# Kernel tuning notes

Measured on AMD Instinct MI355X. Metric: run time of the kernel, lower is better.

Reference implementation:

```python
import jax, jax.numpy as jnp
import numpy as np

B, L, T, IN, H, OUT = 1024, 64, 128, 13, 64, 13
NEG = -1e30


def gru_step(x, h, Wih, Whh, bih, bhh):
    # PyTorch GRU cell: gates ordered (r, z, n)
    gi = x @ Wih.T + bih          # [B, 3H]
    gh = h @ Whh.T + bhh          # [B, 3H]
    ir, iz, inn = jnp.split(gi, 3, axis=-1)
    hr, hz, hn = jnp.split(gh, 3, axis=-1)
    r = jax.nn.sigmoid(ir + hr)
    z = jax.nn.sigmoid(iz + hz)
    n = jnp.tanh(inn + r * hn)
    return (1.0 - z) * n + z * h


def setup_inputs() -> dict:
    key = jax.random.key(0)
    ks = jax.random.split(key, 10)
    s = float(1.0 / np.sqrt(H))
    x = jax.random.normal(ks[0], (B, L, IN), jnp.float32)
    lengths = jax.random.randint(ks[1], (B,), 1, L + 1).at[0].set(L)
    Wih = jax.random.uniform(ks[2], (3 * H, IN), jnp.float32, -s, s)
    Whh = jax.random.uniform(ks[3], (3 * H, H), jnp.float32, -s, s)
    bih = jax.random.uniform(ks[4], (3 * H,), jnp.float32, -s, s)
    bhh = jax.random.uniform(ks[5], (3 * H,), jnp.float32, -s, s)
    Wf = jax.random.uniform(ks[6], (OUT, H), jnp.float32, -s, s)
    bf = jax.random.uniform(ks[7], (OUT,), jnp.float32, -s, s)
    Wa = jax.random.uniform(ks[8], (H, H), jnp.float32, -s, s)
    ba = jax.random.uniform(ks[9], (H,), jnp.float32, -s, s)
    return dict(x=x, lengths=lengths, output_length=T, Wih=Wih, Whh=Whh,
                bih=bih, bhh=bhh, Wf=Wf, bf=bf, Wa=Wa, ba=ba)


def reference(x, lengths, output_length, Wih, Whh, bih, bhh, Wf, bf, Wa, ba):
    b, l = x.shape[0], x.shape[1]
    xT = jnp.swapaxes(x, 0, 1)                        # [L, B, IN]
    h0 = jnp.zeros((b, H), x.dtype)

    # Encoder: masked GRU emulating pack_padded/pad_packed semantics:
    # hidden frozen past each sequence's length; outputs zero past length.
    def enc(h, inp):
        t, xt = inp
        hn = gru_step(xt, h, Wih, Whh, bih, bhh)
        valid = (t < lengths)[:, None]
        h = jnp.where(valid, hn, h)
        return h, jnp.where(valid, hn, 0.0)

    h, outs = jax.lax.scan(enc, h0, (jnp.arange(l), xT))
    # output[:, -1, :] of the padded output (zeros for seqs shorter than max)
    nin = outs[-1] @ Wf.T + bf                        # [B, OUT]

    Tn = output_length
    buf0 = jnp.zeros((Tn, b, H), x.dtype)             # growing past-prediction buffer

    def dec(carry, t):
        h, buf, nin = carry
        hn = gru_step(nin, h, Wih, Whh, bih, bhh)     # output_lstm == hidden (1 layer, 1 step)
        # attention recomputed over all past predictions (softmax over time axis)
        logits = jnp.einsum('tbh,gh->tbg', buf, Wa) + ba      # [T, B, H]
        logits = jnp.where((jnp.arange(Tn) < t)[:, None, None], logits, NEG)
        w = jax.nn.softmax(logits, axis=0)
        o = hn + jnp.sum(w * buf, axis=0)             # at t=0 buffer is all zeros -> +0
        y = o @ Wf.T + bf
        return (hn, buf.at[t].set(o), y), y

    _, ys = jax.lax.scan(dec, (h, buf0, nin), jnp.arange(Tn))
    return jnp.swapaxes(ys, 0, 1)                     # [B, T, OUT]
```

## Files before the change

### kernel.cpp

```cpp
#include <hip/hip_runtime.h>
#include <stdint.h>
#include <math.h>

#define BATCH 1024
#define SEQL  64
#define TDEC  128
#define NIN   13
#define NH    64
#define NOUT  13

typedef _Float16 h2 __attribute__((ext_vector_type(2)));
typedef __fp16   g2 __attribute__((ext_vector_type(2)));

union FU  { uint32_t u; float f; };
union HU  { uint16_t u; _Float16 h; };
union H2U { uint32_t u; h2 h; g2 g; };

__device__ __forceinline__ float bf2f(uint16_t v) { FU t; t.u = ((uint32_t)v) << 16; return t.f; }
__device__ __forceinline__ float hf2f(uint16_t v) { HU t; t.u = v; return (float)t.h; }

__device__ __forceinline__ float ldf(const void* p, long i, int mode) {
    if (mode == 1) return bf2f(((const uint16_t*)p)[i]);
    if (mode == 2) return hf2f(((const uint16_t*)p)[i]);
    return ((const float*)p)[i];
}

__device__ __forceinline__ bool pass_stats(const void* p, int n, int lane, int mode,
                                           float band_lo, float band_hi, float max_ok) {
    int m = (n + 1) / 2;
    int cnt = (m < 64) ? m : 64;
    bool ok_max = true, in_band = false;
    if (lane < cnt) {
        long pos = 2L * (((long)lane * m) / cnt);
        float v = (mode == 1) ? bf2f(((const uint16_t*)p)[pos])
                              : hf2f(((const uint16_t*)p)[pos]);
        float a = fabsf(v);
        ok_max  = (a <= max_ok);
        in_band = (a >= band_lo && a <= band_hi);
    }
    bool allmax = __all(ok_max);
    int nb = (int)__popcll(__ballot(in_band));
    int need = cnt / 4; if (need < 1) need = 1;
    return allmax && (nb >= need);
}
__device__ __forceinline__ int detect(const void* p, int n, int lane,
                                      float band_lo, float band_hi, float max_ok) {
    if (pass_stats(p, n, lane, 1, band_lo, band_hi, max_ok)) return 1;
    if (pass_stats(p, n, lane, 2, band_lo, band_hi, max_ok)) return 2;
    return 0;
}
__device__ __forceinline__ bool detect_len64(const int* p, int lane) {
    int v = p[2 * lane + 1];
    return __all(v == 0);
}

__device__ __forceinline__ float dot2(h2 a, h2 b, float c) {
#if __has_builtin(__builtin_amdgcn_fdot2)
    return __builtin_amdgcn_fdot2(a, b, c, false);
#else
    return c + (float)a[0] * (float)b[0] + (float)a[1] * (float)b[1];
#endif
}
__device__ __forceinline__ uint32_t pku(float a, float b) {
    H2U t; t.g = __builtin_amdgcn_cvt_pkrtz(a, b); return t.u;
}
__device__ __forceinline__ h2 uh(uint32_t u) { H2U t; t.u = u; return t.h; }
__device__ __forceinline__ float rcp_(float x) { return __builtin_amdgcn_rcpf(x); }
__device__ __forceinline__ float exp2_(float x) {
#if __has_builtin(__builtin_amdgcn_exp2f)
    return __builtin_amdgcn_exp2f(x);
#else
    return __expf(x * 0.69314718056f);
#endif
}
__device__ __forceinline__ float sigm2(float xs)  { return rcp_(1.0f + exp2_(-xs)); }
__device__ __forceinline__ float tanh2(float xs)  { return 1.0f - 2.0f * rcp_(exp2_(xs) + 1.0f); }

__device__ __forceinline__ float swap1(float v) {
    FU a; a.f = v;
    FU b; b.u = (uint32_t)__builtin_amdgcn_mov_dpp((int)a.u, 0xB1, 0xF, 0xF, true);
    return b.f;
}

#define BCAST32(vreg, dst)                                                 \
    {                                                                      \
        uint32_t _pr = pku((vreg), swap1(vreg));                           \
        _Pragma("unroll")                                                  \
        for (int _k = 0; _k < 32; ++_k)                                    \
            (dst)[_k] = __builtin_amdgcn_readlane(_pr, 2 * _k);            \
    }

#define BWRITE(DSTB, V)                                                    \
    {                                                                      \
        float _w  = swap1(V);                                              \
        float _lo = odd ? _w  : (V);                                       \
        float _hi = odd ? (V) : _w;                                        \
        (DSTB)[jhalf] = pku(_lo, _hi);                                     \
    }
#define BREAD(SRC, DST)                                                    \
    {                                                                      \
        _Pragma("unroll")                                                  \
        for (int _k = 0; _k < 32; _k += 4) {                               \
            uint4 _q = *(const uint4*)((SRC) + _k);                        \
            (DST)[_k]     = _q.x; (DST)[_k + 1] = _q.y;                    \
            (DST)[_k + 2] = _q.z; (DST)[_k + 3] = _q.w;                    \
        }                                                                  \
    }

__global__ __launch_bounds__(64, 1)
void gru_attn_kernel(const void* __restrict__ x, const int* __restrict__ lengths,
                     const void* __restrict__ Wih, const void* __restrict__ Whh,
                     const void* __restrict__ bih, const void* __restrict__ bhh,
                     const void* __restrict__ Wf, const void* __restrict__ bfv,
                     const void* __restrict__ Wa, const void* __restrict__ ba,
                     float* __restrict__ out)
{
    const int b = blockIdx.x;
    const int j = threadIdx.x;
    const bool odd = j & 1;
    const int jhalf = j >> 1;

    __shared__ __align__(16) uint32_t ob[32];

    const int dX   = detect(x,   BATCH * SEQL * NIN, j, 0.25f, 4.0f, 16.0f);
    const int dWih = detect(Wih, 3 * NH * NIN, j, 0.04f, 0.13f, 0.14f);
    const int dWhh = detect(Whh, 3 * NH * NH,  j, 0.04f, 0.13f, 0.14f);
    const int dBih = detect(bih, 3 * NH,       j, 0.04f, 0.13f, 0.14f);
    const int dBhh = detect(bhh, 3 * NH,       j, 0.04f, 0.13f, 0.14f);
    const int dWf  = detect(Wf,  NOUT * NH,    j, 0.04f, 0.13f, 0.14f);
    const int dBf  = detect(bfv, NOUT,         j, 0.04f, 0.13f, 0.14f);
    const int dWa  = detect(Wa,  NH * NH,      j, 0.04f, 0.13f, 0.14f);
    const int dBa  = detect(ba,  NH,           j, 0.04f, 0.13f, 0.14f);
    const bool len64 = detect_len64(lengths, j);

    const float L2E  = 1.44269504089f;
    const float L2E2 = 2.88539008177f;

    h2 wihr[7], wihz[7], wihn[7];
    h2 whhr[32], whhz[32], whhn[32];
    h2 wap[32], wfp[32];

#pragma unroll
    for (int k = 0; k < 7; ++k) {
        float a0 = ldf(Wih, (0 * NH + j) * NIN + 2 * k, dWih);
        float a1 = (2 * k + 1 < NIN) ? ldf(Wih, (0 * NH + j) * NIN + 2 * k + 1, dWih) : 0.0f;
        wihr[k] = uh(pku(a0 * L2E, a1 * L2E));
        float b0 = ldf(Wih, (1 * NH + j) * NIN + 2 * k, dWih);
        float b1 = (2 * k + 1 < NIN) ? ldf(Wih, (1 * NH + j) * NIN + 2 * k + 1, dWih) : 0.0f;
        wihz[k] = uh(pku(b0 * L2E, b1 * L2E));
        float c0 = ldf(Wih, (2 * NH + j) * NIN + 2 * k, dWih);
        float c1 = (2 * k + 1 < NIN) ? ldf(Wih, (2 * NH + j) * NIN + 2 * k + 1, dWih) : 0.0f;
        wihn[k] = uh(pku(c0 * L2E2, c1 * L2E2));
    }
    const int jf = (j < NOUT) ? j : 0;
#pragma unroll
    for (int k = 0; k < 32; ++k) {
        whhr[k] = uh(pku(ldf(Whh, (0 * NH + j) * NH + 2 * k, dWhh) * L2E,
                         ldf(Whh, (0 * NH + j) * NH + 2 * k + 1, dWhh) * L2E));
        whhz[k] = uh(pku(ldf(Whh, (1 * NH + j) * NH + 2 * k, dWhh) * L2E,
                         ldf(Whh, (1 * NH + j) * NH + 2 * k + 1, dWhh) * L2E));
        whhn[k] = uh(pku(ldf(Whh, (2 * NH + j) * NH + 2 * k, dWhh) * L2E2,
                         ldf(Whh, (2 * NH + j) * NH + 2 * k + 1, dWhh) * L2E2));
        wap[k]  = uh(pku(ldf(Wa, j * NH + 2 * k, dWa) * L2E,
                         ldf(Wa, j * NH + 2 * k + 1, dWa) * L2E));
        wfp[k]  = uh(pku(ldf(Wf, jf * NH + 2 * k, dWf),
                         ldf(Wf, jf * NH + 2 * k + 1, dWf)));
    }

    const float bcr = (ldf(bih, j, dBih)      + ldf(bhh, j, dBhh))      * L2E;
    const float bcz = (ldf(bih, NH + j, dBih) + ldf(bhh, NH + j, dBhh)) * L2E;
    const float bni = ldf(bih, 2 * NH + j, dBih) * L2E2;
    const float bnh = ldf(bhh, 2 * NH + j, dBhh) * L2E2;
    const float baj = ldf(ba, j, dBa) * L2E;
    const float bfj = ldf(bfv, jf, dBf);
    const int len = len64 ? lengths[2 * b] : lengths[b];

    uint32_t xp[7];
    {
        const long base = ((long)b * SEQL + j) * NIN;
        float v[14];
#pragma unroll
        for (int k = 0; k < NIN; ++k) v[k] = ldf(x, base + k, dX);
        v[13] = 0.0f;
#pragma unroll
        for (int p = 0; p < 7; ++p) xp[p] = pku(v[2 * p], v[2 * p + 1]);
    }

    float h = 0.0f;
    float out_last = 0.0f;

    uint32_t hpk[32];
    BCAST32(h, hpk);

#pragma unroll 2
    for (int t = 0; t < SEQL; ++t) {
        uint32_t xw[7];
#pragma unroll
        for (int p = 0; p < 7; ++p) xw[p] = __builtin_amdgcn_readlane(xp[p], t);

        float arA = bcr, azA = bcz, hnA = bnh, anA = bni;
        float arB = 0.0f, azB = 0.0f, hnB = 0.0f;
        float arC = 0.0f, azC = 0.0f, hnC = 0.0f;
        float arD = 0.0f, azD = 0.0f, hnD = 0.0f;
#pragma unroll
        for (int k = 0; k < 32; k += 4) {
            h2 h0 = uh(hpk[k]), h1 = uh(hpk[k + 1]), h2v = uh(hpk[k + 2]), h3 = uh(hpk[k + 3]);
            arA = dot2(whhr[k],     h0, arA); azA = dot2(whhz[k],     h0, azA); hnA = dot2(whhn[k],     h0, hnA);
            arB = dot2(whhr[k + 1], h1, arB); azB = dot2(whhz[k + 1], h1, azB); hnB = dot2(whhn[k + 1], h1, hnB);
            arC = dot2(whhr[k + 2], h2v, arC); azC = dot2(whhz[k + 2], h2v, azC); hnC = dot2(whhn[k + 2], h2v, hnC);
            arD = dot2(whhr[k + 3], h3, arD); azD = dot2(whhz[k + 3], h3, azD); hnD = dot2(whhn[k + 3], h3, hnD);
        }
#pragma unroll
        for (int p = 0; p < 7; ++p) {
            h2 xv = uh(xw[p]);
            arB = dot2(wihr[p], xv, arB);
            azB = dot2(wihz[p], xv, azB);
            anA = dot2(wihn[p], xv, anA);
        }
        float ar = (arA + arB) + (arC + arD);
        float az = (azA + azB) + (azC + azD);
        float hna = (hnA + hnB) + (hnC + hnD);
        float r = sigm2(ar);
        float z = sigm2(az);
        float n = tanh2(anA + r * hna);
        float hnew = n + z * (h - n);
        bool upd = (t < len);
        h = upd ? hnew : h;
        if (t == SEQL - 1) out_last = upd ? hnew : 0.0f;
        BCAST32(h, hpk);
    }

    uint32_t ypk[7];
    {
        uint32_t opk[32];
        BCAST32(out_last, opk);
        float nA = bfj, nB = 0.0f, nC = 0.0f, nD = 0.0f;
#pragma unroll
        for (int k = 0; k < 32; k += 4) {
            nA = dot2(wfp[k],     uh(opk[k]),     nA);
            nB = dot2(wfp[k + 1], uh(opk[k + 1]), nB);
            nC = dot2(wfp[k + 2], uh(opk[k + 2]), nC);
            nD = dot2(wfp[k + 3], uh(opk[k + 3]), nD);
        }
        float nv = (nA + nB) + (nC + nD);
        float nz = (j < NOUT) ? nv : 0.0f;
        uint32_t pr = pku(nz, swap1(nz));
#pragma unroll
        for (int k = 0; k < 7; ++k) ypk[k] = __builtin_amdgcn_readlane(pr, 2 * k);
    }

    float m = -1e30f, Zs = 0.0f, num = 0.0f;
    float o_prev;

    {
        float arA = bcr, azA = bcz, hnA = bnh, anA = bni;
        float arB = 0.0f, azB = 0.0f, hnB = 0.0f;
        float arC = 0.0f, azC = 0.0f, hnC = 0.0f;
        float arD = 0.0f, azD = 0.0f, hnD = 0.0f;
#pragma unroll
        for (int k = 0; k < 32; k += 4) {
            h2 h0 = uh(hpk[k]), h1 = uh(hpk[k + 1]), h2v = uh(hpk[k + 2]), h3 = uh(hpk[k + 3]);
            arA = dot2(whhr[k],     h0, arA); azA = dot2(whhz[k],     h0, azA); hnA = dot2(whhn[k],     h0, hnA);
            arB = dot2(whhr[k + 1], h1, arB); azB = dot2(whhz[k + 1], h1, azB); hnB = dot2(whhn[k + 1], h1, hnB);
            arC = dot2(whhr[k + 2], h2v, arC); azC = dot2(whhz[k + 2], h2v, azC); hnC = dot2(whhn[k + 2], h2v, hnC);
            arD = dot2(whhr[k + 3], h3, arD); azD = dot2(whhz[k + 3], h3, azD); hnD = dot2(whhn[k + 3], h3, hnD);
        }
#pragma unroll
        for (int p = 0; p < 7; ++p) {
            h2 xv = uh(ypk[p]);
            arB = dot2(wihr[p], xv, arB);
            azB = dot2(wihz[p], xv, azB);
            anA = dot2(wihn[p], xv, anA);
        }
        float ar = (arA + arB) + (arC + arD);
        float az = (azA + azB) + (azC + azD);
        float hna = (hnA + hnB) + (hnC + hnD);
        float r = sigm2(ar);
        float z = sigm2(az);
        float n = tanh2(anA + r * hna);
        float hnew = n + z * (h - n);
        h = hnew;
        BCAST32(hnew, hpk);
        o_prev = hnew;
        BWRITE(ob, o_prev);
    }

#pragma unroll 1
    for (int t = 0; t < TDEC - 1; ++t) {
        uint32_t opk[32];
        BREAD(ob, opk);

        float arA = bcr, azA = bcz, hnA = bnh, anA = bni;
        float arB = 0.0f, azB = 0.0f, hnB = 0.0f;
        float arC = 0.0f, azC = 0.0f, hnC = 0.0f;
        float arD = 0.0f, azD = 0.0f, hnD = 0.0f;

#pragma unroll
        for (int k = 0; k < 16; k += 4) {
            h2 h0 = uh(hpk[k]), h1 = uh(hpk[k + 1]), h2v = uh(hpk[k + 2]), h3 = uh(hpk[k + 3]);
            arA = dot2(whhr[k],     h0, arA); azA = dot2(whhz[k],     h0, azA); hnA = dot2(whhn[k],     h0, hnA);
            arB = dot2(whhr[k + 1], h1, arB); azB = dot2(whhz[k + 1], h1, azB); hnB = dot2(whhn[k + 1], h1, hnB);
            arC = dot2(whhr[k + 2], h2v, arC); azC = dot2(whhz[k + 2], h2v, azC); hnC = dot2(whhn[k + 2], h2v, hnC);
            arD = dot2(whhr[k + 3], h3, arD); azD = dot2(whhz[k + 3], h3, azD); hnD = dot2(whhn[k + 3], h3, hnD);
        }

        float sA = baj, sB = 0.0f, sC = 0.0f, sD = 0.0f;
        float yA = bfj, yB = 0.0f, yC = 0.0f, yD = 0.0f;

#pragma unroll
        for (int k = 16; k < 32; k += 4) {
            const int k2 = k - 16;
            h2 h0 = uh(hpk[k]), h1 = uh(hpk[k + 1]), h2v = uh(hpk[k + 2]), h3 = uh(hpk[k + 3]);
            h2 o0 = uh(opk[k2]), o1 = uh(opk[k2 + 1]), o2 = uh(opk[k2 + 2]), o3 = uh(opk[k2 + 3]);
            arA = dot2(whhr[k],     h0, arA); azA = dot2(whhz[k],     h0, azA); hnA = dot2(whhn[k],     h0, hnA);
            sA = dot2(wap[k2],     o0, sA);  yA = dot2(wfp[k2],     o0, yA);
            arB = dot2(whhr[k + 1], h1, arB); azB = dot2(whhz[k + 1], h1, azB); hnB = dot2(whhn[k + 1], h1, hnB);
            sB = dot2(wap[k2 + 1], o1, sB);  yB = dot2(wfp[k2 + 1], o1, yB);
            arC = dot2(whhr[k + 2], h2v, arC); azC = dot2(whhz[k + 2], h2v, azC); hnC = dot2(whhn[k + 2], h2v, hnC);
            sC = dot2(wap[k2 + 2], o2, sC);  yC = dot2(wfp[k2 + 2], o2, yC);
            arD = dot2(whhr[k + 3], h3, arD); azD = dot2(whhz[k + 3], h3, azD); hnD = dot2(whhn[k + 3], h3, hnD);
            sD = dot2(wap[k2 + 3], o3, sD);  yD = dot2(wfp[k2 + 3], o3, yD);
        }

#pragma unroll
        for (int k = 16; k < 32; k += 4) {
            yA = dot2(wfp[k],     uh(opk[k]),     yA);
            yB = dot2(wfp[k + 1], uh(opk[k + 1]), yB);
            yC = dot2(wfp[k + 2], uh(opk[k + 2]), yC);
            yD = dot2(wfp[k + 3], uh(opk[k + 3]), yD);
        }
        float yv = (yA + yB) + (yC + yD);
        {
            float yz = (j < NOUT) ? yv : 0.0f;
            uint32_t pr = pku(yz, swap1(yz));
#pragma unroll
            for (int k = 0; k < 7; ++k) ypk[k] = __builtin_amdgcn_readlane(pr, 2 * k);
        }

#pragma unroll
        for (int k = 16; k < 32; k += 4) {
            sA = dot2(wap[k],     uh(opk[k]),     sA);
            sB = dot2(wap[k + 1], uh(opk[k + 1]), sB);
            sC = dot2(wap[k + 2], uh(opk[k + 2]), sC);
            sD = dot2(wap[k + 3], uh(opk[k + 3]), sD);
        }

#pragma unroll
        for (int p = 0; p < 7; ++p) {
            h2 xv = uh(ypk[p]);
            arB = dot2(wihr[p], xv, arB);
            azB = dot2(wihz[p], xv, azB);
            anA = dot2(wihn[p], xv, anA);
        }

        float s_ = (sA + sB) + (sC + sD);
        float mn = fmaxf(m, s_);
        float al = exp2_(m - mn);
        float pp = exp2_(s_ - mn);
        Zs  = Zs * al + pp;
        num = num * al + pp * o_prev;
        m = mn;
        float attn = num * rcp_(Zs);

        float ar = (arA + arB) + (arC + arD);
        float az = (azA + azB) + (azC + azD);
        float hna = (hnA + hnB) + (hnC + hnD);
        float r_ = sigm2(ar);
        float z_ = sigm2(az);
        float n_ = tanh2(anA + r_ * hna);
        float hnew = n_ + z_ * (h - n_);
        h = hnew;

        float o_ = hnew + attn;
        BCAST32(hnew, hpk);
        BWRITE(ob, o_);
        o_prev = o_;

        if (j < NOUT) out[((size_t)b * TDEC + t) * NOUT + j] = yv;
    }

    {
        uint32_t opk[32];
        BREAD(ob, opk);
        float yA = bfj, yB = 0.0f, yC = 0.0f, yD = 0.0f;
#pragma unroll
        for (int k = 0; k < 32; k += 4) {
            yA = dot2(wfp[k],     uh(opk[k]),     yA);
            yB = dot2(wfp[k + 1], uh(opk[k + 1]), yB);
            yC = dot2(wfp[k + 2], uh(opk[k + 2]), yC);
            yD = dot2(wfp[k + 3], uh(opk[k + 3]), yD);
        }
        float yv = (yA + yB) + (yC + yD);
        if (j < NOUT) out[((size_t)b * TDEC + (TDEC - 1)) * NOUT + j] = yv;
    }
}

extern "C" void kernel_launch(void* const* d_in, const int* in_sizes, int n_in,
                              void* d_out, int out_size, void* d_ws, size_t ws_size,
                              hipStream_t stream) {
    (void)in_sizes; (void)n_in; (void)out_size; (void)d_ws; (void)ws_size;
    const void* x      = d_in[0];
    const int* lengths = (const int*)d_in[1];
    const void* Wih = d_in[3];
    const void* Whh = d_in[4];
    const void* bih = d_in[5];
    const void* bhh = d_in[6];
    const void* Wf  = d_in[7];
    const void* bf  = d_in[8];
    const void* Wa  = d_in[9];
    const void* ba  = d_in[10];
    float* out = (float*)d_out;

    gru_attn_kernel<<<dim3(BATCH), dim3(64), 0, stream>>>(
        x, lengths, Wih, Whh, bih, bhh, Wf, bf, Wa, ba, out);
}
```

Baseline: 218.5 us.

## Fold Wf projection into decoder input weights to remove serial y dependency

Precomputes the combined matrix Wih·Wf (and Wih·bf into the biases) so each decoder step's input gates come straight from the previous output o instead of waiting on the y projection and its broadcast. This takes the y→gate chain off the per-step critical path, but adds three more 32-entry packed weight arrays per thread, so register pressure rises. The hidden state now goes through LDS (BWRITE/BREAD) with a wave barrier instead of the readlane broadcast, and the output store is shifted to the next iteration. Folding the weights in fp16 also changes rounding slightly.

```diff
diff --git a/kernel.cpp b/kernel.cpp
--- a/kernel.cpp
+++ b/kernel.cpp
@@ -75,6 +75,7 @@
 }
 __device__ __forceinline__ float sigm2(float xs)  { return rcp_(1.0f + exp2_(-xs)); }
 __device__ __forceinline__ float tanh2(float xs)  { return 1.0f - 2.0f * rcp_(exp2_(xs) + 1.0f); }
+__device__ __forceinline__ void wb() { __builtin_amdgcn_wave_barrier(); }
 
 __device__ __forceinline__ float swap1(float v) {
     FU a; a.f = v;
@@ -120,6 +121,7 @@
     const bool odd = j & 1;
     const int jhalf = j >> 1;
 
+    __shared__ __align__(16) uint32_t hb[32];
     __shared__ __align__(16) uint32_t ob[32];
 
     const int dX   = detect(x,   BATCH * SEQL * NIN, j, 0.25f, 4.0f, 16.0f);
@@ -136,23 +138,49 @@
     const float L2E  = 1.44269504089f;
     const float L2E2 = 2.88539008177f;
 
+    float wr13[NIN], wz13[NIN], wn13[NIN];
+#pragma unroll
+    for (int i = 0; i < NIN; ++i) {
+        wr13[i] = ldf(Wih, (0 * NH + j) * NIN + i, dWih);
+        wz13[i] = ldf(Wih, (1 * NH + j) * NIN + i, dWih);
+        wn13[i] = ldf(Wih, (2 * NH + j) * NIN + i, dWih);
+    }
+    float fr = 0.0f, fz = 0.0f, fn = 0.0f;
+#pragma unroll
+    for (int i = 0; i < NIN; ++i) {
+        float bfi = ldf(bfv, i, dBf);
+        fr += wr13[i] * bfi; fz += wz13[i] * bfi; fn += wn13[i] * bfi;
+    }
+
+    h2 wcr[32], wcz[32], wcn[32];
+#pragma unroll 4
+    for (int kk = 0; kk < 32; ++kk) {
+        float cr0 = 0.f, cr1 = 0.f, cz0 = 0.f, cz1 = 0.f, cn0 = 0.f, cn1 = 0.f;
+#pragma unroll
+        for (int i = 0; i < NIN; ++i) {
+            float w0 = ldf(Wf, (long)i * NH + 2 * kk, dWf);
+            float w1 = ldf(Wf, (long)i * NH + 2 * kk + 1, dWf);
+            cr0 += wr13[i] * w0; cr1 += wr13[i] * w1;
+            cz0 += wz13[i] * w0; cz1 += wz13[i] * w1;
+            cn0 += wn13[i] * w0; cn1 += wn13[i] * w1;
+        }
+        wcr[kk] = uh(pku(cr0 * L2E,  cr1 * L2E));
+        wcz[kk] = uh(pku(cz0 * L2E,  cz1 * L2E));
+        wcn[kk] = uh(pku(cn0 * L2E2, cn1 * L2E2));
+    }
+
     h2 wihr[7], wihz[7], wihn[7];
-    h2 whhr[32], whhz[32], whhn[32];
-    h2 wap[32], wfp[32];
-
 #pragma unroll
     for (int k = 0; k < 7; ++k) {
-        float a0 = ldf(Wih, (0 * NH + j) * NIN + 2 * k, dWih);
-        float a1 = (2 * k + 1 < NIN) ? ldf(Wih, (0 * NH + j) * NIN + 2 * k + 1, dWih) : 0.0f;
-        wihr[k] = uh(pku(a0 * L2E, a1 * L2E));
-        float b0 = ldf(Wih, (1 * NH + j) * NIN + 2 * k, dWih);
-        float b1 = (2 * k + 1 < NIN) ? ldf(Wih, (1 * NH + j) * NIN + 2 * k + 1, dWih) : 0.0f;
-        wihz[k] = uh(pku(b0 * L2E, b1 * L2E));
-        float c0 = ldf(Wih, (2 * NH + j) * NIN + 2 * k, dWih);
-        float c1 = (2 * k + 1 < NIN) ? ldf(Wih, (2 * NH + j) * NIN + 2 * k + 1, dWih) : 0.0f;
-        wihn[k] = uh(pku(c0 * L2E2, c1 * L2E2));
+        float a1 = (2 * k + 1 < NIN) ? wr13[2 * k + 1] : 0.0f;
+        float b1 = (2 * k + 1 < NIN) ? wz13[2 * k + 1] : 0.0f;
+        float c1 = (2 * k + 1 < NIN) ? wn13[2 * k + 1] : 0.0f;
+        wihr[k] = uh(pku(wr13[2 * k] * L2E,  a1 * L2E));
+        wihz[k] = uh(pku(wz13[2 * k] * L2E,  b1 * L2E));
+        wihn[k] = uh(pku(wn13[2 * k] * L2E2, c1 * L2E2));
     }
     const int jf = (j < NOUT) ? j : 0;
+    h2 whhr[32], whhz[32], whhn[32], wap[32], wfp[32];
 #pragma unroll
     for (int k = 0; k < 32; ++k) {
         whhr[k] = uh(pku(ldf(Whh, (0 * NH + j) * NH + 2 * k, dWhh) * L2E,
@@ -167,10 +195,13 @@
                          ldf(Wf, jf * NH + 2 * k + 1, dWf)));
     }
 
-    const float bcr = (ldf(bih, j, dBih)      + ldf(bhh, j, dBhh))      * L2E;
-    const float bcz = (ldf(bih, NH + j, dBih) + ldf(bhh, NH + j, dBhh)) * L2E;
-    const float bni = ldf(bih, 2 * NH + j, dBih) * L2E2;
-    const float bnh = ldf(bhh, 2 * NH + j, dBhh) * L2E2;
+    const float bcrE = (ldf(bih, j, dBih)      + ldf(bhh, j, dBhh))      * L2E;
+    const float bczE = (ldf(bih, NH + j, dBih) + ldf(bhh, NH + j, dBhh)) * L2E;
+    const float bniE = ldf(bih, 2 * NH + j, dBih) * L2E2;
+    const float bnh  = ldf(bhh, 2 * NH + j, dBhh) * L2E2;
+    const float bcrD = bcrE + fr * L2E;
+    const float bczD = bczE + fz * L2E;
+    const float bniD = bniE + fn * L2E2;
     const float baj = ldf(ba, j, dBa) * L2E;
     const float bfj = ldf(bfv, jf, dBf);
     const int len = len64 ? lengths[2 * b] : lengths[b];
@@ -198,7 +229,7 @@
 #pragma unroll
         for (int p = 0; p < 7; ++p) xw[p] = __builtin_amdgcn_readlane(xp[p], t);
 
-        float arA = bcr, azA = bcz, hnA = bnh, anA = bni;
+        float arA = bcrE, azA = bczE, hnA = bnh, anA = bniE;
         float arB = 0.0f, azB = 0.0f, hnB = 0.0f;
         float arC = 0.0f, azC = 0.0f, hnC = 0.0f;
         float arD = 0.0f, azD = 0.0f, hnD = 0.0f;
@@ -249,11 +280,9 @@
         for (int k = 0; k < 7; ++k) ypk[k] = __builtin_amdgcn_readlane(pr, 2 * k);
     }
 
-    float m = -1e30f, Zs = 0.0f, num = 0.0f;
     float o_prev;
-
     {
-        float arA = bcr, azA = bcz, hnA = bnh, anA = bni;
+        float arA = bcrE, azA = bczE, hnA = bnh, anA = bniE;
         float arB = 0.0f, azB = 0.0f, hnB = 0.0f;
         float arC = 0.0f, azC = 0.0f, hnC = 0.0f;
         float arD = 0.0f, azD = 0.0f, hnD = 0.0f;
@@ -280,24 +309,27 @@
         float n = tanh2(anA + r * hna);
         float hnew = n + z * (h - n);
         h = hnew;
-        BCAST32(hnew, hpk);
         o_prev = hnew;
+        BWRITE(hb, hnew);
         BWRITE(ob, o_prev);
-    }
+        wb();
+    }
+
+    float m = -1e30f, Zs = 0.0f, num = 0.0f;
 
 #pragma unroll 1
-    for (int t = 0; t < TDEC - 1; ++t) {
-        uint32_t opk[32];
-        BREAD(ob, opk);
-
-        float arA = bcr, azA = bcz, hnA = bnh, anA = bni;
-        float arB = 0.0f, azB = 0.0f, hnB = 0.0f;
-        float arC = 0.0f, azC = 0.0f, hnC = 0.0f;
-        float arD = 0.0f, azD = 0.0f, hnD = 0.0f;
-
-#pragma unroll
-        for (int k = 0; k < 16; k += 4) {
-            h2 h0 = uh(hpk[k]), h1 = uh(hpk[k + 1]), h2v = uh(hpk[k + 2]), h3 = uh(hpk[k + 3]);
+    for (int t = 1; t < TDEC; ++t) {
+        uint32_t hv[32], ov[32];
+        BREAD(hb, hv);
+        BREAD(ob, ov);
+
+        float arA = bcrD, azA = bczD, anA = bniD, hnA = bnh;
+        float arB = 0.0f, azB = 0.0f, anB = 0.0f, hnB = 0.0f;
+        float arC = 0.0f, azC = 0.0f, anC = 0.0f, hnC = 0.0f;
+        float arD = 0.0f, azD = 0.0f, anD = 0.0f, hnD = 0.0f;
+#pragma unroll
+        for (int k = 0; k < 32; k += 4) {
+            h2 h0 = uh(hv[k]), h1 = uh(hv[k + 1]), h2v = uh(hv[k + 2]), h3 = uh(hv[k + 3]);
             arA = dot2(whhr[k],     h0, arA); azA = dot2(whhz[k],     h0, azA); hnA = dot2(whhn[k],     h0, hnA);
             arB = dot2(whhr[k + 1], h1, arB); azB = dot2(whhz[k + 1], h1, azB); hnB = dot2(whhn[k + 1], h1, hnB);
             arC = dot2(whhr[k + 2], h2v, arC); azC = dot2(whhz[k + 2], h2v, azC); hnC = dot2(whhn[k + 2], h2v, hnC);
@@ -306,52 +338,21 @@
 
         float sA = baj, sB = 0.0f, sC = 0.0f, sD = 0.0f;
         float yA = bfj, yB = 0.0f, yC = 0.0f, yD = 0.0f;
-
-#pragma unroll
-        for (int k = 16; k < 32; k += 4) {
-            const int k2 = k - 16;
-            h2 h0 = uh(hpk[k]), h1 = uh(hpk[k + 1]), h2v = uh(hpk[k + 2]), h3 = uh(hpk[k + 3]);
-            h2 o0 = uh(opk[k2]), o1 = uh(opk[k2 + 1]), o2 = uh(opk[k2 + 2]), o3 = uh(opk[k2 + 3]);
-            arA = dot2(whhr[k],     h0, arA); azA = dot2(whhz[k],     h0, azA); hnA = dot2(whhn[k],     h0, hnA);
-            sA = dot2(wap[k2],     o0, sA);  yA = dot2(wfp[k2],     o0, yA);
-            arB = dot2(whhr[k + 1], h1, arB); azB = dot2(whhz[k + 1], h1, azB); hnB = dot2(whhn[k + 1], h1, hnB);
-            sB = dot2(wap[k2 + 1], o1, sB);  yB = dot2(wfp[k2 + 1], o1, yB);
-            arC = dot2(whhr[k + 2], h2v, arC); azC = dot2(whhz[k + 2], h2v, azC); hnC = dot2(whhn[k + 2], h2v, hnC);
-            sC = dot2(wap[k2 + 2], o2, sC);  yC = dot2(wfp[k2 + 2], o2, yC);
-            arD = dot2(whhr[k + 3], h3, arD); azD = dot2(whhz[k + 3], h3, azD); hnD = dot2(whhn[k + 3], h3, hnD);
-            sD = dot2(wap[k2 + 3], o3, sD);  yD = dot2(wfp[k2 + 3], o3, yD);
-        }
-
-#pragma unroll
-        for (int k = 16; k < 32; k += 4) {
-            yA = dot2(wfp[k],     uh(opk[k]),     yA);
-            yB = dot2(wfp[k + 1], uh(opk[k + 1]), yB);
-            yC = dot2(wfp[k + 2], uh(opk[k + 2]), yC);
-            yD = dot2(wfp[k + 3], uh(opk[k + 3]), yD);
-        }
+#pragma unroll
+        for (int k = 0; k < 32; k += 4) {
+            h2 o0 = uh(ov[k]), o1 = uh(ov[k + 1]), o2 = uh(ov[k + 2]), o3 = uh(ov[k + 3]);
+            arA = dot2(wcr[k],     o0, arA); azA = dot2(wcz[k],     o0, azA); anA = dot2(wcn[k],     o0, anA);
+            sA  = dot2(wap[k],     o0, sA);  yA  = dot2(wfp[k],     o0, yA);
+            arB = dot2(wcr[k + 1], o1, arB); azB = dot2(wcz[k + 1], o1, azB); anB = dot2(wcn[k + 1], o1, anB);
+            sB  = dot2(wap[k + 1], o1, sB);  yB  = dot2(wfp[k + 1], o1, yB);
+            arC = dot2(wcr[k + 2], o2, arC); azC = dot2(wcz[k + 2], o2, azC); anC = dot2(wcn[k + 2], o2, anC);
+            sC  = dot2(wap[k + 2], o2, sC);  yC  = dot2(wfp[k + 2], o2, yC);
+            arD = dot2(wcr[k + 3], o3, arD); azD = dot2(wcz[k + 3], o3, azD); anD = dot2(wcn[k + 3], o3, anD);
+            sD  = dot2(wap[k + 3], o3, sD);  yD  = dot2(wfp[k + 3], o3, yD);
+        }
+
         float yv = (yA + yB) + (yC + yD);
-        {
-            float yz = (j < NOUT) ? yv : 0.0f;
-            uint32_t pr = pku(yz, swap1(yz));
-#pragma unroll
-            for (int k = 0; k < 7; ++k) ypk[k] = __builtin_amdgcn_readlane(pr, 2 * k);
-        }
-
-#pragma unroll
-        for (int k = 16; k < 32; k += 4) {
-            sA = dot2(wap[k],     uh(opk[k]),     sA);
-            sB = dot2(wap[k + 1], uh(opk[k + 1]), sB);
-            sC = dot2(wap[k + 2], uh(opk[k + 2]), sC);
-            sD = dot2(wap[k + 3], uh(opk[k + 3]), sD);
-        }
-
-#pragma unroll
-        for (int p = 0; p < 7; ++p) {
-            h2 xv = uh(ypk[p]);
-            arB = dot2(wihr[p], xv, arB);
-            azB = dot2(wihz[p], xv, azB);
-            anA = dot2(wihn[p], xv, anA);
-        }
+        if (j < NOUT) out[((size_t)b * TDEC + (t - 1)) * NOUT + j] = yv;
 
         float s_ = (sA + sB) + (sC + sD);
         float mn = fmaxf(m, s_);
@@ -360,35 +361,35 @@
         Zs  = Zs * al + pp;
         num = num * al + pp * o_prev;
         m = mn;
-        float attn = num * rcp_(Zs);
-
-        float ar = (arA + arB) + (arC + arD);
-        float az = (azA + azB) + (azC + azD);
+        float a_ = num * rcp_(Zs);
+
+        float ar  = (arA + arB) + (arC + arD);
+        float az  = (azA + azB) + (azC + azD);
+        float an  = (anA + anB) + (anC + anD);
         float hna = (hnA + hnB) + (hnC + hnD);
         float r_ = sigm2(ar);
         float z_ = sigm2(az);
-        float n_ = tanh2(anA + r_ * hna);
+        float n_ = tanh2(an + r_ * hna);
         float hnew = n_ + z_ * (h - n_);
         h = hnew;
 
-        float o_ = hnew + attn;
-        BCAST32(hnew, hpk);
+        float o_ = hnew + a_;
+        BWRITE(hb, hnew);
         BWRITE(ob, o_);
+        wb();
         o_prev = o_;
-
-        if (j < NOUT) out[((size_t)b * TDEC + t) * NOUT + j] = yv;
     }
 
     {
-        uint32_t opk[32];
-        BREAD(ob, opk);
+        uint32_t ov[32];
+        BREAD(ob, ov);
         float yA = bfj, yB = 0.0f, yC = 0.0f, yD = 0.0f;
 #pragma unroll
         for (int k = 0; k < 32; k += 4) {
-            yA = dot2(wfp[k],     uh(opk[k]),     yA);
-            yB = dot2(wfp[k + 1], uh(opk[k + 1]), yB);
-            yC = dot2(wfp[k + 2], uh(opk[k + 2]), yC);
-            yD = dot2(wfp[k + 3], uh(opk[k + 3]), yD);
+            yA = dot2(wfp[k],     uh(ov[k]),     yA);
+            yB = dot2(wfp[k + 1], uh(ov[k + 1]), yB);
+            yC = dot2(wfp[k + 2], uh(ov[k + 2]), yC);
+            yD = dot2(wfp[k + 3], uh(ov[k + 3]), yD);
         }
         float yv = (yA + yB) + (yC + yD);
         if (j < NOUT) out[((size_t)b * TDEC + (TDEC - 1)) * NOUT + j] = yv;
```

Result: slower. 426.4 us (+95.1%).
